# Optimization experiments

Hardware: AMD Instinct MI355X
Metric: run time of the kernel (lower is better)

The kernel has to match this reference:

```python
import jax, jax.numpy as jnp
import numpy as np

TOP_K = 2

def setup_inputs() -> dict:
    key = jax.random.key(0)
    k1, k2, k3, k4 = jax.random.split(key, 4)
    B, T, C = 4, 2048, 1024
    E, D_FF = 8, 1024  # d_ff = 1 * n_embd
    x = jax.random.normal(k1, (B, T, C), dtype=jnp.float32)
    router_w = jax.random.normal(k2, (E, C), dtype=jnp.float32) * 0.02
    w1 = jax.random.normal(k3, (E, C, D_FF), dtype=jnp.float32) * 0.02
    w2 = jax.random.normal(k4, (E, D_FF, C), dtype=jnp.float32) * 0.02
    return {"x": x, "router_w": router_w, "w1": w1, "w2": w2}

def reference(x, router_w, w1, w2):
    B, T, C = x.shape
    x_flat = x.reshape(-1, C)                          # [N, C]
    logits = x_flat @ router_w.T                       # [N, E]
    probs = jax.nn.softmax(logits, axis=-1)
    weights, indices = jax.lax.top_k(probs, TOP_K)     # [N, K], [N, K]
    # Dense per-expert compute (same math as gathering w1/w2 per token,
    # without duplicating weight slices per token).
    hidden = jax.nn.relu(jnp.einsum('nc,ecf->nef', x_flat, w1))  # [N, E, d_ff]
    out_all = jnp.einsum('nef,efc->nec', hidden, w2)             # [N, E, C]
    sel = jnp.take_along_axis(out_all, indices[:, :, None], axis=1)  # [N, K, C]
    out = jnp.sum(sel * weights[:, :, None], axis=1)   # [N, C]
    return out.reshape(B, T, C)
```

## Files before the change

kernel.cpp:

```cpp
#include <hip/hip_runtime.h>
#include <hip/hip_bf16.h>

#define NTOK 8192
#define CDIM 1024
#define FDIM 1024
#define NEXP 8
#define BM 256
#define BN 256
#define BK 64
#define NKT (CDIM / BK)
#define NWG 384

typedef __attribute__((ext_vector_type(8))) short short8;
typedef __attribute__((ext_vector_type(4))) float f32x4;

union Pack4 { __hip_bfloat16 h[4]; unsigned long long v; };
union U4 { unsigned long long u; unsigned short s[4]; };

typedef const unsigned int __attribute__((address_space(1)))* gas_ptr;
typedef unsigned int __attribute__((address_space(3)))* las_ptr;

__device__ __forceinline__ void gload16(const void* g, void* l) {
    __builtin_amdgcn_global_load_lds(
        (gas_ptr)(unsigned long long)g,
        (las_ptr)(unsigned int)(unsigned long long)l,
        16, 0, 0);
}

__device__ __forceinline__ float bf2f(unsigned short v) {
    unsigned int t = (unsigned int)v << 16;
    return __uint_as_float(t);
}

__global__ __launch_bounds__(256) void router_kernel(
    const float* __restrict__ x, const float* __restrict__ rw,
    __hip_bfloat16* __restrict__ xb,
    int* __restrict__ cnt, int* __restrict__ rows, float* __restrict__ wts,
    int* __restrict__ slotEI)
{
    __shared__ int lcnt[NEXP];
    __shared__ int lt[NEXP][32];
    __shared__ float lw[NEXP][32];
    __shared__ int base[NEXP];
    const int tid = threadIdx.x;
    const int wv = tid >> 6, lane = tid & 63;
    if (tid < NEXP) lcnt[tid] = 0;
    __syncthreads();

    for (int tt = 0; tt < 4; tt++) {
        const int n = blockIdx.x * 16 + wv * 4 + tt;
        float acc[NEXP];
#pragma unroll
        for (int e = 0; e < NEXP; e++) acc[e] = 0.f;
#pragma unroll
        for (int c0 = 0; c0 < CDIM; c0 += 256) {
            const size_t o = (size_t)n * CDIM + c0 + lane * 4;
            float4 xv = *(const float4*)(x + o);
            Pack4 p4;
            p4.h[0] = __float2bfloat16(xv.x); p4.h[1] = __float2bfloat16(xv.y);
            p4.h[2] = __float2bfloat16(xv.z); p4.h[3] = __float2bfloat16(xv.w);
            *(unsigned long long*)(xb + o) = p4.v;
#pragma unroll
            for (int e = 0; e < NEXP; e++) {
                float4 w4 = *(const float4*)&rw[e * CDIM + c0 + lane * 4];
                acc[e] += xv.x * w4.x + xv.y * w4.y + xv.z * w4.z + xv.w * w4.w;
            }
        }
#pragma unroll
        for (int e = 0; e < NEXP; e++) {
#pragma unroll
            for (int s = 32; s > 0; s >>= 1) acc[e] += __shfl_xor(acc[e], s);
        }
        if (lane == 0) {
            float mx = acc[0];
#pragma unroll
            for (int e = 1; e < NEXP; e++) mx = fmaxf(mx, acc[e]);
            float p[NEXP], se = 0.f;
#pragma unroll
            for (int e = 0; e < NEXP; e++) { p[e] = __expf(acc[e] - mx); se += p[e]; }
            float inv = 1.f / se;
            int i0 = 0;
#pragma unroll
            for (int e = 1; e < NEXP; e++) if (p[e] > p[i0]) i0 = e;
            int i1 = (i0 == 0) ? 1 : 0;
#pragma unroll
            for (int e = 0; e < NEXP; e++) if (e != i0 && p[e] > p[i1]) i1 = e;
            int p0 = atomicAdd(&lcnt[i0], 1);
            lt[i0][p0] = n;
            lw[i0][p0] = p[i0] * inv;
            int p1 = atomicAdd(&lcnt[i1], 1);
            lt[i1][p1] = n | (1 << 16);
            lw[i1][p1] = p[i1] * inv;
        }
    }
    __syncthreads();
    if (tid < NEXP) base[tid] = atomicAdd(&cnt[tid * 16], lcnt[tid]);
    __syncthreads();
#pragma unroll
    for (int e = 0; e < NEXP; e++) {
        for (int i = tid; i < lcnt[e]; i += 256) {
            int v = lt[e][i];
            rows[e * NTOK + base[e] + i] = v;
            wts [e * NTOK + base[e] + i] = lw[e][i];
            slotEI[2 * (v & 0xFFFF) + (v >> 16)] = (e << 14) | (base[e] + i);
        }
    }
}

__global__ void scan_offsets(const int* __restrict__ cnt, int* __restrict__ offs,
                             int* __restrict__ wl)
{
    if (threadIdx.x == 0) {
        int s = 0, tF = 0, tR = 0;
        for (int e = 0; e < NEXP; e++) {
            int me = cnt[e * 16];
            offs[e] = s; s += me;
            int m0 = 0;
            for (; m0 + BM <= me; m0 += BM) {
                wl[2 + 2 * tF] = e; wl[3 + 2 * tF] = m0; tF++;
            }
            for (; m0 < me; m0 += 128) {
                wl[160 + 2 * tR] = e; wl[161 + 2 * tR] = m0; tR++;
            }
        }
        wl[0] = tF;
        wl[1] = tR;
    }
}

__global__ __launch_bounds__(256) void transpose_conv(
    const float* __restrict__ src, __hip_bfloat16* __restrict__ dst)
{
    __shared__ float t[64][65];
    const int e = blockIdx.z;
    const int r0 = blockIdx.x * 64, c0 = blockIdx.y * 64;
    const int tid = threadIdx.x;
    const int rr = tid >> 4;
    const int cc = (tid & 15) * 4;
#pragma unroll
    for (int j = 0; j < 4; j++) {
        int row = j * 16 + rr;
        float4 v = *(const float4*)(src + ((size_t)e * 1024 + r0 + row) * 1024 + c0 + cc);
        t[row][cc] = v.x; t[row][cc + 1] = v.y; t[row][cc + 2] = v.z; t[row][cc + 3] = v.w;
    }
    __syncthreads();
#pragma unroll
    for (int j = 0; j < 4; j++) {
        int trow = j * 16 + rr;
        Pack4 o;
#pragma unroll
        for (int k = 0; k < 4; k++) o.h[k] = __float2bfloat16(t[cc + k][trow]);
        *(unsigned long long*)(dst + ((size_t)e * 1024 + c0 + trow) * 1024 + r0 + cc) = o.v;
    }
}

#define STAGE_A(buf, h, kt) { \
    gload16(asrc[2*(h)]   + (kt)*BK, &smem[buf][0][((2*(h))*512   + wv*64)*8]); \
    gload16(asrc[2*(h)+1] + (kt)*BK, &smem[buf][0][((2*(h)+1)*512 + wv*64)*8]); }
#define STAGE_B(buf, h, kt) { \
    gload16(bsrc[2*(h)]   + (kt)*BK, &smem[buf][1][((2*(h))*512   + wv*64)*8]); \
    gload16(bsrc[2*(h)+1] + (kt)*BK, &smem[buf][1][((2*(h)+1)*512 + wv*64)*8]); }
#define PH_READ_A(buf, mh, ks) { \
    const int cs_ = (((ks)*4 + fq) ^ fx) * 8; \
    _Pragma("unroll") \
    for (int i_ = 0; i_ < 4; i_++) \
        af[i_] = *(const short8*)&smem[buf][0][(wr*128 + (mh)*64 + i_*16 + fr)*64 + cs_]; }
#define PH_READ_B(buf, ks) { \
    const int cs_ = (((ks)*4 + fq) ^ fx) * 8; \
    _Pragma("unroll") \
    for (int n_ = 0; n_ < 4; n_++) \
        bfv[n_] = *(const short8*)&smem[buf][1][(wc*64 + n_*16 + fr)*64 + cs_]; }
#define PH_MFMA(mh) { \
    __builtin_amdgcn_s_setprio(1); \
    _Pragma("unroll") \
    for (int i_ = 0; i_ < 4; i_++) \
        _Pragma("unroll") \
        for (int n_ = 0; n_ < 4; n_++) \
            acc[(mh)*4 + i_][n_] = __builtin_amdgcn_mfma_f32_16x16x32_bf16( \
                af[i_], bfv[n_], acc[(mh)*4 + i_][n_], 0, 0, 0); \
    __builtin_amdgcn_s_setprio(0); }
#define SBAR { \
    __builtin_amdgcn_sched_barrier(0); \
    __builtin_amdgcn_s_barrier(); \
    __builtin_amdgcn_sched_barrier(0); }

#define KLOOP_8PHASE \
    STAGE_A(0, 0, 0); STAGE_A(0, 1, 0); STAGE_B(0, 0, 0); STAGE_B(0, 1, 0); \
    STAGE_A(1, 0, 1); \
    asm volatile("s_waitcnt vmcnt(2)" ::: "memory"); \
    SBAR; \
    _Pragma("unroll 1") \
    for (int j = 0; j < NKT / 2; j++) { \
        const int t2 = 2 * j; \
        const bool full = (j < NKT / 2 - 1); \
        short8 af[4], bfv[4]; \
        PH_READ_A(0, 0, 0); PH_READ_B(0, 0); \
        STAGE_A(1, 1, t2 + 1); \
        SBAR; PH_MFMA(0); \
        PH_READ_A(0, 1, 0); \
        STAGE_B(1, 0, t2 + 1); \
        SBAR; PH_MFMA(1); \
        PH_READ_A(0, 0, 1); PH_READ_B(0, 1); \
        STAGE_B(1, 1, t2 + 1); \
        SBAR; PH_MFMA(0); \
        PH_READ_A(0, 1, 1); \
        if (full) { \
            STAGE_A(0, 0, t2 + 2); \
            asm volatile("s_waitcnt vmcnt(2)" ::: "memory"); \
        } else { \
            asm volatile("s_waitcnt vmcnt(0)" ::: "memory"); \
        } \
        SBAR; PH_MFMA(1); \
        PH_READ_A(1, 0, 0); PH_READ_B(1, 0); \
        if (full) STAGE_B(0, 0, t2 + 2); \
        SBAR; PH_MFMA(0); \
        PH_READ_A(1, 1, 0); \
        if (full) STAGE_B(0, 1, t2 + 2); \
        SBAR; PH_MFMA(1); \
        PH_READ_A(1, 0, 1); PH_READ_B(1, 1); \
        if (full) STAGE_A(0, 1, t2 + 2); \
        SBAR; PH_MFMA(0); \
        PH_READ_A(1, 1, 1); \
        if (full) { \
            STAGE_A(1, 0, t2 + 3); \
            asm volatile("s_waitcnt vmcnt(2)" ::: "memory"); \
        } \
        SBAR; PH_MFMA(1); \
    }

__global__ __launch_bounds__(512, 1) void moe_gemm1(
    const __hip_bfloat16* __restrict__ xb, const __hip_bfloat16* __restrict__ w1t,
    const int* __restrict__ cnt, const int* __restrict__ offs,
    const int* __restrict__ wl, const int* __restrict__ rows,
    __hip_bfloat16* __restrict__ hid)
{
    const int bid = blockIdx.x;
    const int tid = threadIdx.x;
    const int lane = tid & 63, wv = tid >> 6;
    const int fr = lane & 15, fq = lane >> 4;
    const int fx = fr & 7;

    __shared__ alignas(16) __hip_bfloat16 smem[2][2][BM * BK];

    const int swz8 = (((tid & 7) ^ ((tid >> 3) & 7))) * 8;

    if (bid < 256) {
        const int wid = (bid & 7) * 32 + (bid >> 3);
        const int t = wid >> 2;
        if (t >= wl[0]) return;
        const int n0 = (wid & 3) * BN;
        const int e = wl[2 + 2 * t], m0 = wl[3 + 2 * t];
        const int off = offs[e];
        const int wr = wv >> 2, wc = wv & 3;

        const __hip_bfloat16* asrc[4];
        const __hip_bfloat16* bsrc[4];
#pragma unroll
        for (int i = 0; i < 4; i++) {
            int row = i * 64 + (tid >> 3);
            int tok = rows[e * NTOK + m0 + row] & 0xFFFF;
            asrc[i] = xb + (size_t)tok * CDIM + swz8;
            bsrc[i] = w1t + ((size_t)e * FDIM + n0 + row) * CDIM + swz8;
        }

        f32x4 acc[8][4] = {};
        KLOOP_8PHASE;
        __syncthreads();

        __hip_bfloat16 (*Cl)[BN] = reinterpret_cast<__hip_bfloat16(*)[BN]>(&smem[0][0][0]);
#pragma unroll
        for (int m = 0; m < 8; m++)
#pragma unroll
            for (int n = 0; n < 4; n++)
#pragma unroll
                for (int r = 0; r < 4; r++) {
                    int il = wr * 128 + m * 16 + fq * 4 + r;
                    float v = acc[m][n][r];
                    Cl[il][wc * 64 + n * 16 + fr] = __float2bfloat16(v > 0.f ? v : 0.f);
                }
        __syncthreads();
#pragma unroll
        for (int i = 0; i < 16; i++) {
            int chunk = i * 512 + tid;
            int row = chunk >> 5, c8 = (chunk & 31) * 8;
            *(short8*)(hid + (size_t)(off + m0 + row) * FDIM + n0 + c8) =
                *(const short8*)&Cl[row][c8];
        }
    } else {
        const int f = bid - 256;
        const int t = f >> 3;
        if (t >= wl[1]) return;
        const int n0 = (f & 7) * 128;
        const int e = wl[160 + 2 * t], m0 = wl[161 + 2 * t];
        const int me = cnt[e * 16], off = offs[e];
        const int wr2 = wv >> 2, wc2 = wv & 3;

        const __hip_bfloat16* asrcF[2];
        const __hip_bfloat16* bsrcF[2];
#pragma unroll
        for (int i = 0; i < 2; i++) {
            int row = i * 64 + (tid >> 3);
            int gi = m0 + row;
            int ri = gi < me ? gi : me - 1;
            int tok = rows[e * NTOK + ri] & 0xFFFF;
            asrcF[i] = xb + (size_t)tok * CDIM + swz8;
            bsrcF[i] = w1t + ((size_t)e * FDIM + n0 + row) * CDIM + swz8;
        }

        f32x4 accF[4][2] = {};

#pragma unroll
        for (int i = 0; i < 2; i++) {
            gload16(asrcF[i], &smem[0][0][(i * 512 + wv * 64) * 8]);
            gload16(bsrcF[i], &smem[0][1][(i * 512 + wv * 64) * 8]);
        }

        int cur = 0;
        for (int kt = 0; kt < NKT; kt++) {
            __builtin_amdgcn_s_barrier();
            if (kt + 1 < NKT) {
                const int k1 = (kt + 1) * BK;
#pragma unroll
                for (int i = 0; i < 2; i++) {
                    gload16(asrcF[i] + k1, &smem[cur ^ 1][0][(i * 512 + wv * 64) * 8]);
                    gload16(bsrcF[i] + k1, &smem[cur ^ 1][1][(i * 512 + wv * 64) * 8]);
                }
                asm volatile("s_waitcnt vmcnt(4)" ::: "memory");
            } else {
                asm volatile("s_waitcnt vmcnt(0)" ::: "memory");
            }
            __builtin_amdgcn_s_barrier();
            __builtin_amdgcn_sched_barrier(0);
#pragma unroll
            for (int ks = 0; ks < 2; ks++) {
                short8 afF[4], bfF[2];
                const int cs = ((ks * 4 + fq) ^ fx) * 8;
#pragma unroll
                for (int m = 0; m < 4; m++)
                    afF[m] = *(const short8*)&smem[cur][0][(wr2 * 64 + m * 16 + fr) * 64 + cs];
#pragma unroll
                for (int n = 0; n < 2; n++)
                    bfF[n] = *(const short8*)&smem[cur][1][(wc2 * 32 + n * 16 + fr) * 64 + cs];
#pragma unroll
                for (int m = 0; m < 4; m++)
#pragma unroll
                    for (int n = 0; n < 2; n++)
                        accF[m][n] = __builtin_amdgcn_mfma_f32_16x16x32_bf16(
                            afF[m], bfF[n], accF[m][n], 0, 0, 0);
            }
            cur ^= 1;
        }
        __syncthreads();

        __hip_bfloat16 (*Cl)[128] = reinterpret_cast<__hip_bfloat16(*)[128]>(&smem[0][0][0]);
#pragma unroll
        for (int m = 0; m < 4; m++)
#pragma unroll
            for (int n = 0; n < 2; n++)
#pragma unroll
                for (int r = 0; r < 4; r++) {
                    int il = wr2 * 64 + m * 16 + fq * 4 + r;
                    float v = accF[m][n][r];
                    Cl[il][wc2 * 32 + n * 16 + fr] = __float2bfloat16(v > 0.f ? v : 0.f);
                }
        __syncthreads();
#pragma unroll
        for (int i = 0; i < 4; i++) {
            int chunk = i * 512 + tid;
            int row = chunk >> 4, c8 = (chunk & 15) * 8;
            int gi = m0 + row;
            if (gi < me)
                *(short8*)(hid + (size_t)(off + gi) * FDIM + n0 + c8) =
                    *(const short8*)&Cl[row][c8];
        }
    }
}

__global__ __launch_bounds__(512, 1) void moe_gemm2(
    const __hip_bfloat16* __restrict__ hid, const __hip_bfloat16* __restrict__ w2t,
    const int* __restrict__ cnt, const int* __restrict__ offs,
    const int* __restrict__ wl, const int* __restrict__ rows,
    const float* __restrict__ wts, __hip_bfloat16* __restrict__ ybuf,
    float* __restrict__ out)
{
    const int bid = blockIdx.x;
    const int tid = threadIdx.x;
    const int lane = tid & 63, wv = tid >> 6;
    const int fr = lane & 15, fq = lane >> 4;
    const int fx = fr & 7;

    __shared__ alignas(16) __hip_bfloat16 smem[2][2][BM * BK];
    __shared__ int rtok[BM];
    __shared__ float rwt[BM];

    const int swz8 = (((tid & 7) ^ ((tid >> 3) & 7))) * 8;

    if (bid < 256) {
        const int wid = (bid & 7) * 32 + (bid >> 3);
        const int t = wid >> 2;
        if (t >= wl[0]) return;
        const int n0 = (wid & 3) * BN;
        const int e = wl[2 + 2 * t], m0 = wl[3 + 2 * t];
        const int off = offs[e];
        const int wr = wv >> 2, wc = wv & 3;

        if (tid < BM) {
            rtok[tid] = rows[e * NTOK + m0 + tid] & 0xFFFF;
            rwt[tid] = wts[e * NTOK + m0 + tid];
        }
        __syncthreads();

        const __hip_bfloat16* asrc[4];
        const __hip_bfloat16* bsrc[4];
#pragma unroll
        for (int i = 0; i < 4; i++) {
            int row = i * 64 + (tid >> 3);
            asrc[i] = hid + (size_t)(off + m0 + row) * FDIM + swz8;
            bsrc[i] = w2t + ((size_t)e * CDIM + n0 + row) * FDIM + swz8;
        }

        f32x4 acc[8][4] = {};
        KLOOP_8PHASE;
        __syncthreads();

        if (ybuf) {
            __hip_bfloat16 (*Cl)[BN] = reinterpret_cast<__hip_bfloat16(*)[BN]>(&smem[0][0][0]);
#pragma unroll
            for (int m = 0; m < 8; m++)
#pragma unroll
                for (int n = 0; n < 4; n++)
#pragma unroll
                    for (int r = 0; r < 4; r++) {
                        int il = wr * 128 + m * 16 + fq * 4 + r;
                        Cl[il][wc * 64 + n * 16 + fr] =
                            __float2bfloat16(rwt[il] * acc[m][n][r]);
                    }
            __syncthreads();
#pragma unroll
            for (int i = 0; i < 16; i++) {
                int chunk = i * 512 + tid;
                int row = chunk >> 5, c8 = (chunk & 31) * 8;
                *(short8*)(ybuf + (size_t)(off + m0 + row) * CDIM + n0 + c8) =
                    *(const short8*)&Cl[row][c8];
            }
        } else {
#pragma unroll
            for (int m = 0; m < 8; m++)
#pragma unroll
                for (int n = 0; n < 4; n++)
#pragma unroll
                    for (int r = 0; r < 4; r++) {
                        int il = wr * 128 + m * 16 + fq * 4 + r;
                        atomicAdd(&out[(size_t)rtok[il] * CDIM + n0 + wc * 64 + n * 16 + fr],
                                  rwt[il] * acc[m][n][r]);
                    }
        }
    } else {
        const int f = bid - 256;
        const int t = f >> 3;
        if (t >= wl[1]) return;
        const int n0 = (f & 7) * 128;
        const int e = wl[160 + 2 * t], m0 = wl[161 + 2 * t];
        const int me = cnt[e * 16], off = offs[e];
        const int wr2 = wv >> 2, wc2 = wv & 3;

        if (tid < 128) {
            int gi = m0 + tid;
            int ri = gi < me ? gi : me - 1;
            rtok[tid] = rows[e * NTOK + ri] & 0xFFFF;
            rwt[tid] = gi < me ? wts[e * NTOK + ri] : 0.f;
        }
        __syncthreads();

        const __hip_bfloat16* asrcF[2];
        const __hip_bfloat16* bsrcF[2];
#pragma unroll
        for (int i = 0; i < 2; i++) {
            int row = i * 64 + (tid >> 3);
            int gi = m0 + row;
            int ri = gi < me ? gi : me - 1;
            asrcF[i] = hid + (size_t)(off + ri) * FDIM + swz8;
            bsrcF[i] = w2t + ((size_t)e * CDIM + n0 + row) * FDIM + swz8;
        }

        f32x4 accF[4][2] = {};

#pragma unroll
        for (int i = 0; i < 2; i++) {
            gload16(asrcF[i], &smem[0][0][(i * 512 + wv * 64) * 8]);
            gload16(bsrcF[i], &smem[0][1][(i * 512 + wv * 64) * 8]);
        }

        int cur = 0;
        for (int kt = 0; kt < NKT; kt++) {
            __builtin_amdgcn_s_barrier();
            if (kt + 1 < NKT) {
                const int k1 = (kt + 1) * BK;
#pragma unroll
                for (int i = 0; i < 2; i++) {
                    gload16(asrcF[i] + k1, &smem[cur ^ 1][0][(i * 512 + wv * 64) * 8]);
                    gload16(bsrcF[i] + k1, &smem[cur ^ 1][1][(i * 512 + wv * 64) * 8]);
                }
                asm volatile("s_waitcnt vmcnt(4)" ::: "memory");
            } else {
                asm volatile("s_waitcnt vmcnt(0)" ::: "memory");
            }
            __builtin_amdgcn_s_barrier();
            __builtin_amdgcn_sched_barrier(0);
#pragma unroll
            for (int ks = 0; ks < 2; ks++) {
                short8 afF[4], bfF[2];
                const int cs = ((ks * 4 + fq) ^ fx) * 8;
#pragma unroll
                for (int m = 0; m < 4; m++)
                    afF[m] = *(const short8*)&smem[cur][0][(wr2 * 64 + m * 16 + fr) * 64 + cs];
#pragma unroll
                for (int n = 0; n < 2; n++)
                    bfF[n] = *(const short8*)&smem[cur][1][(wc2 * 32 + n * 16 + fr) * 64 + cs];
#pragma unroll
                for (int m = 0; m < 4; m++)
#pragma unroll
                    for (int n = 0; n < 2; n++)
                        accF[m][n] = __builtin_amdgcn_mfma_f32_16x16x32_bf16(
                            afF[m], bfF[n], accF[m][n], 0, 0, 0);
            }
            cur ^= 1;
        }
        __syncthreads();

        if (ybuf) {
            __hip_bfloat16 (*Cl)[128] = reinterpret_cast<__hip_bfloat16(*)[128]>(&smem[0][0][0]);
#pragma unroll
            for (int m = 0; m < 4; m++)
#pragma unroll
                for (int n = 0; n < 2; n++)
#pragma unroll
                    for (int r = 0; r < 4; r++) {
                        int il = wr2 * 64 + m * 16 + fq * 4 + r;
                        Cl[il][wc2 * 32 + n * 16 + fr] =
                            __float2bfloat16(rwt[il] * accF[m][n][r]);
                    }
            __syncthreads();
#pragma unroll
            for (int i = 0; i < 4; i++) {
                int chunk = i * 512 + tid;
                int row = chunk >> 4, c8 = (chunk & 15) * 8;
                int gi = m0 + row;
                if (gi < me)
                    *(short8*)(ybuf + (size_t)(off + gi) * CDIM + n0 + c8) =
                        *(const short8*)&Cl[row][c8];
            }
        } else {
#pragma unroll
            for (int m = 0; m < 4; m++)
#pragma unroll
                for (int n = 0; n < 2; n++)
#pragma unroll
                    for (int r = 0; r < 4; r++) {
                        int il = wr2 * 64 + m * 16 + fq * 4 + r;
                        int gi = m0 + il;
                        if (gi < me)
                            atomicAdd(&out[(size_t)rtok[il] * CDIM + n0 + wc2 * 32 + n * 16 + fr],
                                      rwt[il] * accF[m][n][r]);
                    }
        }
    }
}

__global__ __launch_bounds__(256) void gather_out(
    const __hip_bfloat16* __restrict__ yb, const int* __restrict__ slotEI,
    const int* __restrict__ offs, float* __restrict__ out)
{
    for (int n = blockIdx.x; n < NTOK; n += gridDim.x) {
        const int v0 = slotEI[2 * n], v1 = slotEI[2 * n + 1];
        const int s0 = offs[v0 >> 14] + (v0 & 0x3FFF);
        const int s1 = offs[v1 >> 14] + (v1 & 0x3FFF);
        const int c = threadIdx.x * 4;
        U4 a, b;
        a.u = *(const unsigned long long*)(yb + (size_t)s0 * CDIM + c);
        b.u = *(const unsigned long long*)(yb + (size_t)s1 * CDIM + c);
        float4 o;
        o.x = bf2f(a.s[0]) + bf2f(b.s[0]);
        o.y = bf2f(a.s[1]) + bf2f(b.s[1]);
        o.z = bf2f(a.s[2]) + bf2f(b.s[2]);
        o.w = bf2f(a.s[3]) + bf2f(b.s[3]);
        *(float4*)(out + (size_t)n * CDIM + c) = o;
    }
}

extern "C" void kernel_launch(void* const* d_in, const int* in_sizes, int n_in,
                              void* d_out, int out_size, void* d_ws, size_t ws_size,
                              hipStream_t stream)
{
    const float* x  = (const float*)d_in[0];
    const float* rw = (const float*)d_in[1];
    const float* w1 = (const float*)d_in[2];
    const float* w2 = (const float*)d_in[3];
    float* out = (float*)d_out;
    char* ws = (char*)d_ws;

    int* cnt  = (int*)ws;
    int* offs = (int*)(ws + 1024);
    int* wl   = (int*)(ws + 2048);
    int* rows = (int*)(ws + 4096);
    float* wts = (float*)(ws + 4096 + NEXP * NTOK * 4);
    int* slotEI = (int*)(ws + 4096 + 2 * NEXP * NTOK * 4);
    __hip_bfloat16* xb  = (__hip_bfloat16*)(ws + (1u << 20));
    __hip_bfloat16* w1t = (__hip_bfloat16*)(ws + (17u << 20));
    __hip_bfloat16* hid = (__hip_bfloat16*)(ws + (33u << 20));
    __hip_bfloat16* w2t = w1t;
    const bool big = ws_size >= ((size_t)98 << 20);
    __hip_bfloat16* ybuf = big ? (__hip_bfloat16*)(ws + (65u << 20)) : nullptr;

    hipMemsetAsync(cnt, 0, 1024, stream);
    if (!big)
        hipMemsetAsync(d_out, 0, (size_t)out_size * sizeof(float), stream);

    router_kernel<<<NTOK / 16, 256, 0, stream>>>(x, rw, xb, cnt, rows, wts, slotEI);
    scan_offsets<<<1, 64, 0, stream>>>(cnt, offs, wl);
    transpose_conv<<<dim3(16, 16, NEXP), 256, 0, stream>>>(w1, w1t);
    moe_gemm1<<<NWG, 512, 0, stream>>>(xb, w1t, cnt, offs, wl, rows, hid);
    transpose_conv<<<dim3(16, 16, NEXP), 256, 0, stream>>>(w2, w2t);
    moe_gemm2<<<NWG, 512, 0, stream>>>(hid, w2t, cnt, offs, wl, rows, wts, ybuf, out);
    if (big)
        gather_out<<<2048, 256, 0, stream>>>(ybuf, slotEI, offs, out);
}
```

Baseline: 149.2 us.

## Drop scan kernel, fuse weight transposes, restage K-loop loads by operand

Removes the single-thread scan_offsets launch; each GEMM block now derives its expert tile and offset directly from the per-expert counts, and gather_out computes prefix offsets inline. When the workspace is large enough, the two weight transpose kernels merge into one launch with separate buffers for w1t and w2t. The y buffer reuses the xb region to fit the smaller workspace threshold. The 8-phase K loop is also reordered to issue A and B stages in pairs with vmcnt(4) waits. This trades fewer launches and serial gaps for redundant per-block count scans and a different load/compute interleave.

New measurement: 143.8 us. -3.6%, faster.

```diff
diff --git a/kernel.cpp b/kernel.cpp
--- a/kernel.cpp
+++ b/kernel.cpp
@@ -30,6 +30,32 @@
 __device__ __forceinline__ float bf2f(unsigned short v) {
     unsigned int t = (unsigned int)v << 16;
     return __uint_as_float(t);
+}
+
+__device__ __forceinline__ bool find_full_tile(const int* __restrict__ cnt, int tIdx,
+                                               int& e, int& m0, int& off) {
+    int acc = 0, s = 0;
+    for (int ee = 0; ee < NEXP; ee++) {
+        int me = cnt[ee * 16];
+        int nf = me >> 8;
+        if (tIdx < acc + nf) { e = ee; m0 = (tIdx - acc) << 8; off = s; return true; }
+        acc += nf; s += me;
+    }
+    return false;
+}
+__device__ __forceinline__ bool find_fill_tile(const int* __restrict__ cnt, int tIdx,
+                                               int& e, int& m0, int& off, int& me_out) {
+    int acc = 0, s = 0;
+    for (int ee = 0; ee < NEXP; ee++) {
+        int me = cnt[ee * 16];
+        int base = (me >> 8) << 8;
+        int nr = (me - base + 127) >> 7;
+        if (tIdx < acc + nr) {
+            e = ee; m0 = base + ((tIdx - acc) << 7); off = s; me_out = me; return true;
+        }
+        acc += nr; s += me;
+    }
+    return false;
 }
 
 __global__ __launch_bounds__(256) void router_kernel(
@@ -107,24 +133,33 @@
     }
 }
 
-__global__ void scan_offsets(const int* __restrict__ cnt, int* __restrict__ offs,
-                             int* __restrict__ wl)
+__global__ __launch_bounds__(256) void transpose_both(
+    const float* __restrict__ w1, const float* __restrict__ w2,
+    __hip_bfloat16* __restrict__ w1t, __hip_bfloat16* __restrict__ w2t)
 {
-    if (threadIdx.x == 0) {
-        int s = 0, tF = 0, tR = 0;
-        for (int e = 0; e < NEXP; e++) {
-            int me = cnt[e * 16];
-            offs[e] = s; s += me;
-            int m0 = 0;
-            for (; m0 + BM <= me; m0 += BM) {
-                wl[2 + 2 * tF] = e; wl[3 + 2 * tF] = m0; tF++;
-            }
-            for (; m0 < me; m0 += 128) {
-                wl[160 + 2 * tR] = e; wl[161 + 2 * tR] = m0; tR++;
-            }
-        }
-        wl[0] = tF;
-        wl[1] = tR;
+    __shared__ float t[64][65];
+    const int z = blockIdx.z;
+    const float* src = (z < 8) ? w1 : w2;
+    __hip_bfloat16* dst = (z < 8) ? w1t : w2t;
+    const int e = z & 7;
+    const int r0 = blockIdx.x * 64, c0 = blockIdx.y * 64;
+    const int tid = threadIdx.x;
+    const int rr = tid >> 4;
+    const int cc = (tid & 15) * 4;
+#pragma unroll
+    for (int j = 0; j < 4; j++) {
+        int row = j * 16 + rr;
+        float4 v = *(const float4*)(src + ((size_t)e * 1024 + r0 + row) * 1024 + c0 + cc);
+        t[row][cc] = v.x; t[row][cc + 1] = v.y; t[row][cc + 2] = v.z; t[row][cc + 3] = v.w;
+    }
+    __syncthreads();
+#pragma unroll
+    for (int j = 0; j < 4; j++) {
+        int trow = j * 16 + rr;
+        Pack4 o;
+#pragma unroll
+        for (int k = 0; k < 4; k++) o.h[k] = __float2bfloat16(t[cc + k][trow]);
+        *(unsigned long long*)(dst + ((size_t)e * 1024 + c0 + trow) * 1024 + r0 + cc) = o.v;
     }
 }
 
@@ -186,52 +221,55 @@
 
 #define KLOOP_8PHASE \
     STAGE_A(0, 0, 0); STAGE_A(0, 1, 0); STAGE_B(0, 0, 0); STAGE_B(0, 1, 0); \
-    STAGE_A(1, 0, 1); \
-    asm volatile("s_waitcnt vmcnt(2)" ::: "memory"); \
+    STAGE_B(1, 0, 1); STAGE_B(1, 1, 1); \
+    asm volatile("s_waitcnt vmcnt(4)" ::: "memory"); \
     SBAR; \
     _Pragma("unroll 1") \
     for (int j = 0; j < NKT / 2; j++) { \
         const int t2 = 2 * j; \
         const bool full = (j < NKT / 2 - 1); \
         short8 af[4], bfv[4]; \
+         \
         PH_READ_A(0, 0, 0); PH_READ_B(0, 0); \
-        STAGE_A(1, 1, t2 + 1); \
+        STAGE_A(1, 0, t2 + 1); STAGE_A(1, 1, t2 + 1); \
         SBAR; PH_MFMA(0); \
+         \
         PH_READ_A(0, 1, 0); \
-        STAGE_B(1, 0, t2 + 1); \
         SBAR; PH_MFMA(1); \
+         \
         PH_READ_A(0, 0, 1); PH_READ_B(0, 1); \
-        STAGE_B(1, 1, t2 + 1); \
         SBAR; PH_MFMA(0); \
+         \
         PH_READ_A(0, 1, 1); \
         if (full) { \
-            STAGE_A(0, 0, t2 + 2); \
-            asm volatile("s_waitcnt vmcnt(2)" ::: "memory"); \
+            STAGE_B(0, 0, t2 + 2); STAGE_B(0, 1, t2 + 2); \
+            asm volatile("s_waitcnt vmcnt(4)" ::: "memory"); \
         } else { \
             asm volatile("s_waitcnt vmcnt(0)" ::: "memory"); \
         } \
         SBAR; PH_MFMA(1); \
+         \
         PH_READ_A(1, 0, 0); PH_READ_B(1, 0); \
-        if (full) STAGE_B(0, 0, t2 + 2); \
+        if (full) { STAGE_A(0, 0, t2 + 2); STAGE_A(0, 1, t2 + 2); } \
         SBAR; PH_MFMA(0); \
+         \
         PH_READ_A(1, 1, 0); \
-        if (full) STAGE_B(0, 1, t2 + 2); \
         SBAR; PH_MFMA(1); \
+         \
         PH_READ_A(1, 0, 1); PH_READ_B(1, 1); \
-        if (full) STAGE_A(0, 1, t2 + 2); \
         SBAR; PH_MFMA(0); \
+         \
         PH_READ_A(1, 1, 1); \
         if (full) { \
-            STAGE_A(1, 0, t2 + 3); \
-            asm volatile("s_waitcnt vmcnt(2)" ::: "memory"); \
+            STAGE_B(1, 0, t2 + 3); STAGE_B(1, 1, t2 + 3); \
+            asm volatile("s_waitcnt vmcnt(4)" ::: "memory"); \
         } \
         SBAR; PH_MFMA(1); \
     }
 
 __global__ __launch_bounds__(512, 1) void moe_gemm1(
     const __hip_bfloat16* __restrict__ xb, const __hip_bfloat16* __restrict__ w1t,
-    const int* __restrict__ cnt, const int* __restrict__ offs,
-    const int* __restrict__ wl, const int* __restrict__ rows,
+    const int* __restrict__ cnt, const int* __restrict__ rows,
     __hip_bfloat16* __restrict__ hid)
 {
     const int bid = blockIdx.x;
@@ -247,10 +285,9 @@
     if (bid < 256) {
         const int wid = (bid & 7) * 32 + (bid >> 3);
         const int t = wid >> 2;
-        if (t >= wl[0]) return;
+        int e, m0, off;
+        if (!find_full_tile(cnt, t, e, m0, off)) return;
         const int n0 = (wid & 3) * BN;
-        const int e = wl[2 + 2 * t], m0 = wl[3 + 2 * t];
-        const int off = offs[e];
         const int wr = wv >> 2, wc = wv & 3;
 
         const __hip_bfloat16* asrc[4];
@@ -289,10 +326,9 @@
     } else {
         const int f = bid - 256;
         const int t = f >> 3;
-        if (t >= wl[1]) return;
+        int e, m0, off, me;
+        if (!find_fill_tile(cnt, t, e, m0, off, me)) return;
         const int n0 = (f & 7) * 128;
-        const int e = wl[160 + 2 * t], m0 = wl[161 + 2 * t];
-        const int me = cnt[e * 16], off = offs[e];
         const int wr2 = wv >> 2, wc2 = wv & 3;
 
         const __hip_bfloat16* asrcF[2];
@@ -378,8 +414,7 @@
 
 __global__ __launch_bounds__(512, 1) void moe_gemm2(
     const __hip_bfloat16* __restrict__ hid, const __hip_bfloat16* __restrict__ w2t,
-    const int* __restrict__ cnt, const int* __restrict__ offs,
-    const int* __restrict__ wl, const int* __restrict__ rows,
+    const int* __restrict__ cnt, const int* __restrict__ rows,
     const float* __restrict__ wts, __hip_bfloat16* __restrict__ ybuf,
     float* __restrict__ out)
 {
@@ -398,10 +433,9 @@
     if (bid < 256) {
         const int wid = (bid & 7) * 32 + (bid >> 3);
         const int t = wid >> 2;
-        if (t >= wl[0]) return;
+        int e, m0, off;
+        if (!find_full_tile(cnt, t, e, m0, off)) return;
         const int n0 = (wid & 3) * BN;
-        const int e = wl[2 + 2 * t], m0 = wl[3 + 2 * t];
-        const int off = offs[e];
         const int wr = wv >> 2, wc = wv & 3;
 
         if (tid < BM) {
@@ -458,10 +492,9 @@
     } else {
         const int f = bid - 256;
         const int t = f >> 3;
-        if (t >= wl[1]) return;
+        int e, m0, off, me;
+        if (!find_fill_tile(cnt, t, e, m0, off, me)) return;
         const int n0 = (f & 7) * 128;
-        const int e = wl[160 + 2 * t], m0 = wl[161 + 2 * t];
-        const int me = cnt[e * 16], off = offs[e];
         const int wr2 = wv >> 2, wc2 = wv & 3;
 
         if (tid < 128) {
@@ -569,12 +602,17 @@
 
 __global__ __launch_bounds__(256) void gather_out(
     const __hip_bfloat16* __restrict__ yb, const int* __restrict__ slotEI,
-    const int* __restrict__ offs, float* __restrict__ out)
+    const int* __restrict__ cnt, float* __restrict__ out)
 {
     for (int n = blockIdx.x; n < NTOK; n += gridDim.x) {
         const int v0 = slotEI[2 * n], v1 = slotEI[2 * n + 1];
-        const int s0 = offs[v0 >> 14] + (v0 & 0x3FFF);
-        const int s1 = offs[v1 >> 14] + (v1 & 0x3FFF);
+        int e0 = v0 >> 14, e1 = v1 >> 14;
+        int s0 = v0 & 0x3FFF, s1 = v1 & 0x3FFF;
+        for (int ee = 0; ee < NEXP; ee++) {
+            int me = cnt[ee * 16];
+            if (ee < e0) s0 += me;
+            if (ee < e1) s1 += me;
+        }
         const int c = threadIdx.x * 4;
         U4 a, b;
         a.u = *(const unsigned long long*)(yb + (size_t)s0 * CDIM + c);
@@ -600,28 +638,36 @@
     char* ws = (char*)d_ws;
 
     int* cnt  = (int*)ws;
-    int* offs = (int*)(ws + 1024);
-    int* wl   = (int*)(ws + 2048);
     int* rows = (int*)(ws + 4096);
     float* wts = (float*)(ws + 4096 + NEXP * NTOK * 4);
     int* slotEI = (int*)(ws + 4096 + 2 * NEXP * NTOK * 4);
-    __hip_bfloat16* xb  = (__hip_bfloat16*)(ws + (1u << 20));
-    __hip_bfloat16* w1t = (__hip_bfloat16*)(ws + (17u << 20));
-    __hip_bfloat16* hid = (__hip_bfloat16*)(ws + (33u << 20));
-    __hip_bfloat16* w2t = w1t;
-    const bool big = ws_size >= ((size_t)98 << 20);
-    __hip_bfloat16* ybuf = big ? (__hip_bfloat16*)(ws + (65u << 20)) : nullptr;
 
     hipMemsetAsync(cnt, 0, 1024, stream);
-    if (!big)
+
+    const bool big = ws_size >= ((size_t)81 << 20);
+    if (big) {
+        __hip_bfloat16* xb  = (__hip_bfloat16*)(ws + (1u << 20));
+        __hip_bfloat16* w1t = (__hip_bfloat16*)(ws + (17u << 20));
+        __hip_bfloat16* w2t = (__hip_bfloat16*)(ws + (33u << 20));
+        __hip_bfloat16* hid = (__hip_bfloat16*)(ws + (49u << 20));
+        __hip_bfloat16* ybuf = (__hip_bfloat16*)(ws + (1u << 20));
+
+        router_kernel<<<NTOK / 16, 256, 0, stream>>>(x, rw, xb, cnt, rows, wts, slotEI);
+        transpose_both<<<dim3(16, 16, 16), 256, 0, stream>>>(w1, w2, w1t, w2t);
+        moe_gemm1<<<NWG, 512, 0, stream>>>(xb, w1t, cnt, rows, hid);
+        moe_gemm2<<<NWG, 512, 0, stream>>>(hid, w2t, cnt, rows, wts, ybuf, out);
+        gather_out<<<2048, 256, 0, stream>>>(ybuf, slotEI, cnt, out);
+    } else {
+        __hip_bfloat16* xb  = (__hip_bfloat16*)(ws + (1u << 20));
+        __hip_bfloat16* w1t = (__hip_bfloat16*)(ws + (17u << 20));
+        __hip_bfloat16* hid = (__hip_bfloat16*)(ws + (33u << 20));
+        __hip_bfloat16* w2t = w1t;
+
         hipMemsetAsync(d_out, 0, (size_t)out_size * sizeof(float), stream);
-
-    router_kernel<<<NTOK / 16, 256, 0, stream>>>(x, rw, xb, cnt, rows, wts, slotEI);
-    scan_offsets<<<1, 64, 0, stream>>>(cnt, offs, wl);
-    transpose_conv<<<dim3(16, 16, NEXP), 256, 0, stream>>>(w1, w1t);
-    moe_gemm1<<<NWG, 512, 0, stream>>>(xb, w1t, cnt, offs, wl, rows, hid);
-    transpose_conv<<<dim3(16, 16, NEXP), 256, 0, stream>>>(w2, w2t);
-    moe_gemm2<<<NWG, 512, 0, stream>>>(hid, w2t, cnt, offs, wl, rows, wts, ybuf, out);
-    if (big)
-        gather_out<<<2048, 256, 0, stream>>>(ybuf, slotEI, offs, out);
-}
+        router_kernel<<<NTOK / 16, 256, 0, stream>>>(x, rw, xb, cnt, rows, wts, slotEI);
+        transpose_conv<<<dim3(16, 16, NEXP), 256, 0, stream>>>(w1, w1t);
+        moe_gemm1<<<NWG, 512, 0, stream>>>(xb, w1t, cnt, rows, hid);
+        transpose_conv<<<dim3(16, 16, NEXP), 256, 0, stream>>>(w2, w2t);
+        moe_gemm2<<<NWG, 512, 0, stream>>>(hid, w2t, cnt, rows, wts, nullptr, out);
+    }
+}
```
